# Kernel optimization log

Hardware: AMD Instinct MI355X
Metric: run time of the kernel (lower is better)

Reference implementation:

```python
import jax, jax.numpy as jnp
import numpy as np

N_NODES = 200000
N_EDGES = 500000
N_RELS = 256
D = 256  # rnn_in_dim == rnn_hid_dim


def setup_inputs() -> dict:
    key = jax.random.key(0)
    ks = jax.random.split(key, 8)
    src_nid = jax.random.randint(ks[0], (N_EDGES,), 0, N_NODES, dtype=jnp.int32)
    dst_nid = jax.random.randint(ks[1], (N_EDGES,), 0, N_NODES, dtype=jnp.int32)
    rel = jax.random.randint(ks[2], (N_EDGES,), 0, N_RELS, dtype=jnp.int32)
    static_entity_emb = jax.random.normal(ks[3], (N_NODES, D), dtype=jnp.float32)
    dynamic_relation_emb = jax.random.normal(ks[4], (N_RELS, 1, D, 2), dtype=jnp.float32)
    s = 1.0 / np.sqrt(D)
    W_ih = jax.random.uniform(ks[5], (3 * D, D), jnp.float32, -s, s)
    W_hh = jax.random.uniform(ks[6], (3 * D, D), jnp.float32, -s, s)
    kb1, kb2 = jax.random.split(ks[7])
    b_ih = jax.random.uniform(kb1, (3 * D,), jnp.float32, -s, s)
    b_hh = jax.random.uniform(kb2, (3 * D,), jnp.float32, -s, s)
    return {"src_nid": src_nid, "dst_nid": dst_nid, "rel": rel,
            "static_entity_emb": static_entity_emb,
            "dynamic_relation_emb": dynamic_relation_emb,
            "W_ih": W_ih, "W_hh": W_hh, "b_ih": b_ih, "b_hh": b_hh}


def _segment_mean(x, ids, num_segments):
    # x: [E, D], ids: [E] -> [R, D] mean per relation (0 where empty, as scatter_mean)
    sums = jax.ops.segment_sum(x, ids, num_segments=num_segments)
    cnts = jax.ops.segment_sum(jnp.ones((ids.shape[0],), x.dtype), ids,
                               num_segments=num_segments)
    return sums / jnp.maximum(cnts, 1.0)[:, None]


def _gru_cell(x, h, W_ih, W_hh, b_ih, b_hh):
    # PyTorch GRU cell, single step. x,h: [R, H]
    gi = x @ W_ih.T + b_ih            # [R, 3H]
    gh = h @ W_hh.T + b_hh            # [R, 3H]
    i_r, i_z, i_n = jnp.split(gi, 3, axis=-1)
    h_r, h_z, h_n = jnp.split(gh, 3, axis=-1)
    r = jax.nn.sigmoid(i_r + h_r)
    z = jax.nn.sigmoid(i_z + h_z)
    n = jnp.tanh(i_n + r * h_n)
    return (1.0 - z) * n + z * h


def reference(src_nid, dst_nid, rel, static_entity_emb, dynamic_relation_emb,
              W_ih, W_hh, b_ih, b_hh):
    R = dynamic_relation_emb.shape[0]
    # gather node embeddings by edge endpoints, mean-reduce per relation
    src_avg = _segment_mean(static_entity_emb[src_nid], rel, R)  # [R, D]
    dst_avg = _segment_mean(static_entity_emb[dst_nid], rel, R)  # [R, D]
    h_src = dynamic_relation_emb[:, 0, :, 0]  # num_layers==1 -> [R, H]
    h_dst = dynamic_relation_emb[:, 0, :, 1]
    new_src = _gru_cell(src_avg, h_src, W_ih, W_hh, b_ih, b_hh)
    new_dst = _gru_cell(dst_avg, h_dst, W_ih, W_hh, b_ih, b_hh)
    # [R, num_layers=1, H, 2]
    return jnp.stack([new_src, new_dst], axis=-1)[:, None, :, :]
```

## Files before the change

kernel.cpp:

```cpp
#include <hip/hip_runtime.h>
#include <math.h>

#define D 256
#define R 256
#define DIMC 32
#define NODE_CHUNKS 64

__device__ __forceinline__ float sigmoidf(float x) {
    return 1.0f / (1.0f + expf(-x));
}

__global__ void zero_f(float* p, int n) {
    int i = blockIdx.x * blockDim.x + threadIdx.x;
    if (i < n) p[i] = 0.0f;
}
__global__ void zero_i(int* p, int n) {
    int i = blockIdx.x * blockDim.x + threadIdx.x;
    if (i < n) p[i] = 0;
}

__global__ __launch_bounds__(256) void hist_rel(const int* __restrict__ rel,
                                                int E, float* __restrict__ counts) {
    __shared__ int h[R];
    h[threadIdx.x] = 0;
    __syncthreads();
    for (int e = blockIdx.x * blockDim.x + threadIdx.x; e < E;
         e += gridDim.x * blockDim.x)
        atomicAdd(&h[rel[e]], 1);
    __syncthreads();
    atomicAdd(&counts[threadIdx.x], (float)h[threadIdx.x]);
}

__global__ __launch_bounds__(256) void hist_nodes(const int* __restrict__ src,
                                                  const int* __restrict__ dst,
                                                  int E, int* __restrict__ cnt) {
    int i = blockIdx.x * blockDim.x + threadIdx.x;
    if (i < 2 * E) {
        int n = (i < E) ? src[i] : dst[i - E];
        atomicAdd(&cnt[n], 1);
    }
}

__global__ __launch_bounds__(1024) void scan1(const int* __restrict__ cnt, int N,
                                              int* __restrict__ offs,
                                              int* __restrict__ bsum) {
    __shared__ int s[1024];
    int t = threadIdx.x, i = blockIdx.x * 1024 + t;
    int x = (i < N) ? cnt[i] : 0;
    s[t] = x;
    __syncthreads();
    for (int o = 1; o < 1024; o <<= 1) {
        int v = (t >= o) ? s[t - o] : 0;
        __syncthreads();
        s[t] += v;
        __syncthreads();
    }
    if (i < N) offs[i] = s[t] - x;
    if (t == 1023) bsum[blockIdx.x] = s[t];
}
__global__ __launch_bounds__(1024) void scan2(const int* __restrict__ bsum, int NB,
                                              int* __restrict__ bexcl) {
    __shared__ int s[1024];
    int t = threadIdx.x;
    int x = (t < NB) ? bsum[t] : 0;
    s[t] = x;
    __syncthreads();
    for (int o = 1; o < 1024; o <<= 1) {
        int v = (t >= o) ? s[t - o] : 0;
        __syncthreads();
        s[t] += v;
        __syncthreads();
    }
    if (t < NB) bexcl[t] = s[t] - x;
}
__global__ __launch_bounds__(1024) void scan3(int* __restrict__ offs, int N,
                                              const int* __restrict__ bexcl,
                                              int total) {
    int t = threadIdx.x, i = blockIdx.x * 1024 + t;
    if (i < N) offs[i] += bexcl[blockIdx.x];
    if (i == 0) offs[N] = total;
}

__global__ __launch_bounds__(256) void build_pay(const int* __restrict__ src,
                                                 const int* __restrict__ dst,
                                                 const int* __restrict__ rel, int E,
                                                 const int* __restrict__ offs,
                                                 int* __restrict__ cursor,
                                                 unsigned short* __restrict__ pay) {
    int i = blockIdx.x * blockDim.x + threadIdx.x;
    if (i >= 2 * E) return;
    int side = (i >= E) ? 1 : 0;
    int e = side ? i - E : i;
    int n = side ? dst[e] : src[e];
    int r = rel[e];
    int pos = offs[n] + atomicAdd(&cursor[n], 1);
    pay[pos] = (unsigned short)(r | (side << 8));
}

__global__ __launch_bounds__(256) void node_accum(const float* __restrict__ emb,
                                                  const int* __restrict__ offs,
                                                  const unsigned short* __restrict__ pay,
                                                  float* __restrict__ src_sum,
                                                  float* __restrict__ dst_sum,
                                                  int N, int npb) {
    __shared__ float acc[2 * R * DIMC];
    const int tid = threadIdx.x;
    for (int i = tid; i < 2 * R * DIMC; i += 256) acc[i] = 0.0f;
    __syncthreads();

    const int dimbase = blockIdx.y * DIMC;
    const int wave = tid >> 6, lane = tid & 63;
    const int half = lane >> 5, m = lane & 31;
    const int n0 = blockIdx.x * npb;
    const int n1 = (n0 + npb < N) ? (n0 + npb) : N;

    int n = n0 + wave * 2;
    float v = 0.0f;
    if (n + half < n1) v = emb[(size_t)(n + half) * D + dimbase + m];
    for (; n < n1; n += 8) {
        int nA = n + half;
        float vnext = 0.0f;
        int nn = n + 8 + half;
        if (nn < n1) vnext = emb[(size_t)nn * D + dimbase + m];
        if (nA < n1) {
            int oA = offs[nA];
            int cA = offs[nA + 1] - oA;
            for (int k = 0; k < cA; k++) {
                int p = pay[oA + k];
                int r = p & 255, side = p >> 8;
                atomicAdd(&acc[(side << 13) + (r << 5) + m], v);
            }
        }
        v = vnext;
    }
    __syncthreads();
    for (int i = tid; i < 2 * R * DIMC; i += 256) {
        int side = i >> 13, r = (i >> 5) & 255, mm = i & 31;
        float* g = side ? dst_sum : src_sum;
        atomicAdd(&g[r * D + dimbase + mm], acc[i]);
    }
}

__global__ __launch_bounds__(256) void gru_kernel(
    const float* __restrict__ src_sum, const float* __restrict__ dst_sum,
    const float* __restrict__ counts, const float* __restrict__ dyn,
    const float* __restrict__ W_ih, const float* __restrict__ W_hh,
    const float* __restrict__ b_ih, const float* __restrict__ b_hh,
    float* __restrict__ out) {
    __shared__ float xs[D], xd[D], hs[D], hd[D];
    const int r = blockIdx.x, t = threadIdx.x;
    float inv = 1.0f / fmaxf(counts[r], 1.0f);
    xs[t] = src_sum[r * D + t] * inv;
    xd[t] = dst_sum[r * D + t] * inv;
    float h_s = dyn[(r * D + t) * 2 + 0];
    float h_d = dyn[(r * D + t) * 2 + 1];
    hs[t] = h_s;
    hd[t] = h_d;
    __syncthreads();

    float gis[3], gid[3], ghs[3], ghd[3];
#pragma unroll
    for (int g = 0; g < 3; g++) {
        int row = g * D + t;
        const float4* wi = (const float4*)(W_ih + (size_t)row * D);
        const float4* wh = (const float4*)(W_hh + (size_t)row * D);
        float ais = 0.f, aid = 0.f, ahs = 0.f, ahd = 0.f;
        for (int k = 0; k < D / 4; k++) {
            float4 a = wi[k];
            float4 b = wh[k];
            int k4 = k * 4;
            ais += a.x * xs[k4] + a.y * xs[k4 + 1] + a.z * xs[k4 + 2] + a.w * xs[k4 + 3];
            aid += a.x * xd[k4] + a.y * xd[k4 + 1] + a.z * xd[k4 + 2] + a.w * xd[k4 + 3];
            ahs += b.x * hs[k4] + b.y * hs[k4 + 1] + b.z * hs[k4 + 2] + b.w * hs[k4 + 3];
            ahd += b.x * hd[k4] + b.y * hd[k4 + 1] + b.z * hd[k4 + 2] + b.w * hd[k4 + 3];
        }
        float bi = b_ih[row];
        float bh = b_hh[row];
        gis[g] = ais + bi; gid[g] = aid + bi;
        ghs[g] = ahs + bh; ghd[g] = ahd + bh;
    }
    float rs = sigmoidf(gis[0] + ghs[0]);
    float zs = sigmoidf(gis[1] + ghs[1]);
    float ns = tanhf(gis[2] + rs * ghs[2]);
    float new_s = (1.0f - zs) * ns + zs * h_s;

    float rd = sigmoidf(gid[0] + ghd[0]);
    float zd = sigmoidf(gid[1] + ghd[1]);
    float nd = tanhf(gid[2] + rd * ghd[2]);
    float new_d = (1.0f - zd) * nd + zd * h_d;

    out[(r * D + t) * 2 + 0] = new_s;
    out[(r * D + t) * 2 + 1] = new_d;
}

extern "C" void kernel_launch(void* const* d_in, const int* in_sizes, int n_in,
                              void* d_out, int out_size, void* d_ws, size_t ws_size,
                              hipStream_t stream) {
    const int* src_nid = (const int*)d_in[0];
    const int* dst_nid = (const int*)d_in[1];
    const int* rel     = (const int*)d_in[2];
    const float* emb   = (const float*)d_in[3];
    const float* dyn   = (const float*)d_in[4];
    const float* W_ih  = (const float*)d_in[5];
    const float* W_hh  = (const float*)d_in[6];
    const float* b_ih  = (const float*)d_in[7];
    const float* b_hh  = (const float*)d_in[8];
    float* out = (float*)d_out;
    const int E = in_sizes[0];
    const int N = in_sizes[3] / D;

    float* ws      = (float*)d_ws;
    float* src_sum = ws;
    float* dst_sum = ws + R * D;
    float* counts  = ws + 2 * R * D;
    const int nzf  = 2 * R * D + R;
    int* cnt    = (int*)(ws + nzf);
    int* cursor = cnt + N;
    int* offs   = cursor + N;
    int* bsum   = offs + N + 1;
    int* bexcl  = bsum + 1024;
    unsigned short* pay = (unsigned short*)(bexcl + 1024);

    const int NB  = (N + 1023) / 1024;
    const int npb = (N + NODE_CHUNKS - 1) / NODE_CHUNKS;

    zero_f<<<(nzf + 255) / 256, 256, 0, stream>>>(ws, nzf);
    zero_i<<<(2 * N + 255) / 256, 256, 0, stream>>>(cnt, 2 * N);
    hist_rel<<<256, 256, 0, stream>>>(rel, E, counts);
    hist_nodes<<<(2 * E + 255) / 256, 256, 0, stream>>>(src_nid, dst_nid, E, cnt);
    scan1<<<NB, 1024, 0, stream>>>(cnt, N, offs, bsum);
    scan2<<<1, 1024, 0, stream>>>(bsum, NB, bexcl);
    scan3<<<NB, 1024, 0, stream>>>(offs, N, bexcl, 2 * E);
    build_pay<<<(2 * E + 255) / 256, 256, 0, stream>>>(src_nid, dst_nid, rel, E,
                                                       offs, cursor, pay);
    node_accum<<<dim3(NODE_CHUNKS, D / DIMC), 256, 0, stream>>>(
        emb, offs, pay, src_sum, dst_sum, N, npb);
    gru_kernel<<<R, 256, 0, stream>>>(src_sum, dst_sum, counts, dyn, W_ih, W_hh,
                                      b_ih, b_hh, out);
}
```

Baseline: 1.688 ms.

## Partition accumulation over edge payloads instead of nodes with batched gathers

The payload now packs node id, side and relation into a 32-bit word. The accumulation kernel splits work evenly over the node-sorted payload array instead of over node ranges. Each wave loads 64 payloads, broadcasts them with shuffles and issues 16 independent embedding loads before the shared-memory atomics, which exposes more memory-level parallelism and evens out the per-node degree imbalance. In exchange the payload array is twice as large, and a node's embedding row is loaded once per edge instead of once per node.

```diff
diff --git a/kernel.cpp b/kernel.cpp
--- a/kernel.cpp
+++ b/kernel.cpp
@@ -4,7 +4,7 @@
 #define D 256
 #define R 256
 #define DIMC 32
-#define NODE_CHUNKS 64
+#define PCHUNKS 64
 
 __device__ __forceinline__ float sigmoidf(float x) {
     return 1.0f / (1.0f + expf(-x));
@@ -86,7 +86,7 @@
                                                  const int* __restrict__ rel, int E,
                                                  const int* __restrict__ offs,
                                                  int* __restrict__ cursor,
-                                                 unsigned short* __restrict__ pay) {
+                                                 unsigned int* __restrict__ pay) {
     int i = blockIdx.x * blockDim.x + threadIdx.x;
     if (i >= 2 * E) return;
     int side = (i >= E) ? 1 : 0;
@@ -94,15 +94,12 @@
     int n = side ? dst[e] : src[e];
     int r = rel[e];
     int pos = offs[n] + atomicAdd(&cursor[n], 1);
-    pay[pos] = (unsigned short)(r | (side << 8));
-}
-
-__global__ __launch_bounds__(256) void node_accum(const float* __restrict__ emb,
-                                                  const int* __restrict__ offs,
-                                                  const unsigned short* __restrict__ pay,
-                                                  float* __restrict__ src_sum,
-                                                  float* __restrict__ dst_sum,
-                                                  int N, int npb) {
+    pay[pos] = ((unsigned int)n << 9) | ((unsigned int)side << 8) | (unsigned int)r;
+}
+
+__global__ __launch_bounds__(256) void pay_accum(
+    const float* __restrict__ emb, const unsigned int* __restrict__ pay,
+    float* __restrict__ src_sum, float* __restrict__ dst_sum, int M, int ppb) {
     __shared__ float acc[2 * R * DIMC];
     const int tid = threadIdx.x;
     for (int i = tid; i < 2 * R * DIMC; i += 256) acc[i] = 0.0f;
@@ -111,27 +108,45 @@
     const int dimbase = blockIdx.y * DIMC;
     const int wave = tid >> 6, lane = tid & 63;
     const int half = lane >> 5, m = lane & 31;
-    const int n0 = blockIdx.x * npb;
-    const int n1 = (n0 + npb < N) ? (n0 + npb) : N;
-
-    int n = n0 + wave * 2;
-    float v = 0.0f;
-    if (n + half < n1) v = emb[(size_t)(n + half) * D + dimbase + m];
-    for (; n < n1; n += 8) {
-        int nA = n + half;
-        float vnext = 0.0f;
-        int nn = n + 8 + half;
-        if (nn < n1) vnext = emb[(size_t)nn * D + dimbase + m];
-        if (nA < n1) {
-            int oA = offs[nA];
-            int cA = offs[nA + 1] - oA;
-            for (int k = 0; k < cA; k++) {
-                int p = pay[oA + k];
-                int r = p & 255, side = p >> 8;
-                atomicAdd(&acc[(side << 13) + (r << 5) + m], v);
+    const int start = blockIdx.x * ppb;
+    const int end = (start + ppb < M) ? (start + ppb) : M;
+
+    for (int base = start + wave * 64; base < end; base += 256) {
+        int cnt = end - base;
+        if (cnt > 64) cnt = 64;
+        unsigned int p = 0;
+        if (lane < cnt) p = pay[base + lane];
+        if (cnt == 64) {
+#pragma unroll
+            for (int j = 0; j < 32; j += 16) {
+                unsigned int pe[16];
+                float v[16];
+#pragma unroll
+                for (int jj = 0; jj < 16; jj++) {
+                    pe[jj] = __shfl(p, 2 * (j + jj) + half);
+                    int n = pe[jj] >> 9;
+                    v[jj] = emb[(size_t)n * D + dimbase + m];
+                }
+#pragma unroll
+                for (int jj = 0; jj < 16; jj++) {
+                    int idx = (((pe[jj] >> 8) & 1) << 13) | ((pe[jj] & 255) << 5) | m;
+                    atomicAdd(&acc[idx], v[jj]);
+                }
+            }
+        } else {
+            int steps = (cnt + 1) >> 1;
+            for (int j = 0; j < steps; j++) {
+                int e = 2 * j + half;
+                int valid = e < cnt;
+                unsigned int pe = __shfl(p, valid ? e : 0);
+                int n = pe >> 9;
+                float v = emb[(size_t)n * D + dimbase + m];
+                if (valid) {
+                    int idx = (((pe >> 8) & 1) << 13) | ((pe & 255) << 5) | m;
+                    atomicAdd(&acc[idx], v);
+                }
             }
         }
-        v = vnext;
     }
     __syncthreads();
     for (int i = tid; i < 2 * R * DIMC; i += 256) {
@@ -208,6 +223,7 @@
     float* out = (float*)d_out;
     const int E = in_sizes[0];
     const int N = in_sizes[3] / D;
+    const int M = 2 * E;
 
     float* ws      = (float*)d_ws;
     float* src_sum = ws;
@@ -219,22 +235,22 @@
     int* offs   = cursor + N;
     int* bsum   = offs + N + 1;
     int* bexcl  = bsum + 1024;
-    unsigned short* pay = (unsigned short*)(bexcl + 1024);
+    unsigned int* pay = (unsigned int*)(bexcl + 1024);
 
     const int NB  = (N + 1023) / 1024;
-    const int npb = (N + NODE_CHUNKS - 1) / NODE_CHUNKS;
+    const int ppb = (M + PCHUNKS - 1) / PCHUNKS;
 
     zero_f<<<(nzf + 255) / 256, 256, 0, stream>>>(ws, nzf);
     zero_i<<<(2 * N + 255) / 256, 256, 0, stream>>>(cnt, 2 * N);
     hist_rel<<<256, 256, 0, stream>>>(rel, E, counts);
-    hist_nodes<<<(2 * E + 255) / 256, 256, 0, stream>>>(src_nid, dst_nid, E, cnt);
+    hist_nodes<<<(M + 255) / 256, 256, 0, stream>>>(src_nid, dst_nid, E, cnt);
     scan1<<<NB, 1024, 0, stream>>>(cnt, N, offs, bsum);
     scan2<<<1, 1024, 0, stream>>>(bsum, NB, bexcl);
-    scan3<<<NB, 1024, 0, stream>>>(offs, N, bexcl, 2 * E);
-    build_pay<<<(2 * E + 255) / 256, 256, 0, stream>>>(src_nid, dst_nid, rel, E,
-                                                       offs, cursor, pay);
-    node_accum<<<dim3(NODE_CHUNKS, D / DIMC), 256, 0, stream>>>(
-        emb, offs, pay, src_sum, dst_sum, N, npb);
+    scan3<<<NB, 1024, 0, stream>>>(offs, N, bexcl, M);
+    build_pay<<<(M + 255) / 256, 256, 0, stream>>>(src_nid, dst_nid, rel, E,
+                                                   offs, cursor, pay);
+    pay_accum<<<dim3(PCHUNKS, D / DIMC), 256, 0, stream>>>(
+        emb, pay, src_sum, dst_sum, M, ppb);
     gru_kernel<<<R, 256, 0, stream>>>(src_sum, dst_sum, counts, dyn, W_ih, W_hh,
                                       b_ih, b_hh, out);
 }
```

Result: no change. 1.715 ms (+1.5%).
